# Optimization experiments

Hardware: AMD Instinct MI355X
Metric: run time of the kernel (lower is better)

Reference implementation:

```python
import jax, jax.numpy as jnp
import numpy as np

N_NODES = 100000
N_EDGES = 3200000
IN_CH = 256


def setup_inputs() -> dict:
    key = jax.random.key(0)
    k1, k2, k3 = jax.random.split(key, 3)
    x = jax.random.normal(k1, (N_NODES, IN_CH), dtype=jnp.float32)
    edge_index = jax.random.randint(k2, (2, N_EDGES), 0, N_NODES, dtype=jnp.int64)
    # GCNConv linear: weight [in_channels, 1] (applied as x @ W), bias [1]
    W = jax.random.normal(k3, (IN_CH, 1), dtype=jnp.float32) * (1.0 / np.sqrt(IN_CH))
    b = jnp.zeros((1,), dtype=jnp.float32)
    return {"x": x, "edge_index": edge_index, "W": W, "b": b}


def reference(x, edge_index, W, b):
    # PyG GCNConv(in, 1): h = x @ W; add self-loops; symmetric norm; scatter-add to target; + bias
    N = x.shape[0]
    self_loops = jnp.broadcast_to(jnp.arange(N, dtype=edge_index.dtype)[None, :], (2, N))
    ei = jnp.concatenate([edge_index, self_loops], axis=1)  # [2, E+N]
    src, dst = ei[0], ei[1]

    # degree computed at target (col) with unit edge weights, incl. self-loops
    deg = jax.ops.segment_sum(jnp.ones(ei.shape[1], dtype=x.dtype), dst, num_segments=N)
    deg_inv_sqrt = jnp.where(deg > 0, jax.lax.rsqrt(deg), 0.0)
    norm = deg_inv_sqrt[src] * deg_inv_sqrt[dst]  # [E+N]

    h = x @ W  # [N, 1] — project first (out_channels < in_channels)
    msg = norm[:, None] * h[src]  # [E+N, 1]
    out = jax.ops.segment_sum(msg, dst, num_segments=N)  # [N, 1]
    return out + b
```

## Files before the change

kernel.cpp:

```cpp
#include <hip/hip_runtime.h>

#define GCN_N 100000
#define GCN_E 3200000
#define GCN_C 256
#define BSHIFT 8
#define NBUCK 391
#define BCAP 9216

#define NPB 512
#define TPB 1024
#define ROWS ((GCN_N + NPB - 1) / NPB)

#define TB 1024
#define CHUNK 6144
#define NBIN ((GCN_E + CHUNK - 1) / CHUNK)
#define EPT (CHUNK / TB)

__global__ void __launch_bounds__(TPB) k_proj_init(const float* __restrict__ x,
                                                   const float* __restrict__ W,
                                                   float* __restrict__ h,
                                                   int* __restrict__ cursor) {
    const int tid = threadIdx.x, blk = blockIdx.x;
    if (blk == 0) {
        for (int i = tid; i < NBUCK; i += TPB) cursor[i] = 0;
    }
    const int lane = tid & 63, wv = tid >> 6;
    const int r0 = blk * ROWS;
    const int r1 = min(r0 + ROWS, GCN_N);
    const float4 wf = *reinterpret_cast<const float4*>(W + lane * 4);
    for (int i = r0 + wv; i < r1; i += 16) {
        const float4 xv = *reinterpret_cast<const float4*>(x + (size_t)i * GCN_C + lane * 4);
        float s = xv.x * wf.x + xv.y * wf.y + xv.z * wf.z + xv.w * wf.w;
        #pragma unroll
        for (int off = 32; off > 0; off >>= 1) s += __shfl_down(s, off, 64);
        if (lane == 0) h[i] = s;
    }
}

__global__ void __launch_bounds__(TB) k_bin(const int* __restrict__ src,
                                            const int* __restrict__ dst,
                                            int* __restrict__ cursor,
                                            int* __restrict__ bpack) {
    __shared__ int A[CHUNK];
    __shared__ int B[CHUNK];
    __shared__ int hist[NBUCK];
    __shared__ int lscan[NBUCK];
    __shared__ int gbase[NBUCK];
    __shared__ int wsum[16], woff[16];
    const int tid = threadIdx.x, blk = blockIdx.x;
    const int lane = tid & 63, wv = tid >> 6;
    const int c0 = blk * CHUNK;
    const int cn = min(CHUNK, GCN_E - c0);

    for (int b = tid; b < NBUCK; b += TB) hist[b] = 0;

    const int nq = cn >> 2;
    for (int k4 = tid; k4 < nq; k4 += TB) {
        const int4 d = *reinterpret_cast<const int4*>(dst + c0 + k4 * 4);
        const int4 s = *reinterpret_cast<const int4*>(src + c0 + k4 * 4);
        *reinterpret_cast<int4*>(&A[k4 * 4]) = d;
        *reinterpret_cast<int4*>(&B[k4 * 4]) = s;
    }
    for (int k = (cn & ~3) + tid; k < cn; k += TB) {
        A[k] = dst[c0 + k];
        B[k] = src[c0 + k];
    }
    __syncthreads();

    int my_pack[EPT], my_b[EPT], my_off[EPT];
    #pragma unroll
    for (int j = 0; j < EPT; ++j) {
        const int k = tid + j * TB;
        my_b[j] = -1;
        if (k < cn) {
            const int d = A[k];
            const int s = B[k];
            const int b = d >> BSHIFT;
            my_pack[j] = (s << BSHIFT) | (d & 255);
            my_b[j]    = b;
            my_off[j]  = atomicAdd(&hist[b], 1);
        }
    }
    __syncthreads();

    if (tid < NBUCK) gbase[tid] = atomicAdd(&cursor[tid], hist[tid]);
    {
        const int v = (tid < NBUCK) ? hist[tid] : 0;
        int incl = v;
        #pragma unroll
        for (int d2 = 1; d2 < 64; d2 <<= 1) {
            const int t = __shfl_up(incl, d2, 64);
            if (lane >= d2) incl += t;
        }
        if (lane == 63 && wv < 7) wsum[wv] = incl;
        __syncthreads();
        if (tid == 0) { int s = 0; for (int k2 = 0; k2 < 7; ++k2) { woff[k2] = s; s += wsum[k2]; } }
        __syncthreads();
        if (tid < NBUCK) lscan[tid] = incl - v + woff[wv];
    }
    __syncthreads();

    #pragma unroll
    for (int j = 0; j < EPT; ++j) {
        if (my_b[j] >= 0) {
            const int b    = my_b[j];
            const int slot = lscan[b] + my_off[j];
            const int goff = gbase[b] + my_off[j];
            B[slot] = my_pack[j];
            A[slot] = (goff < BCAP) ? (b * BCAP + goff) : -1;
        }
    }
    __syncthreads();

    for (int i = tid; i < cn; i += TB) {
        const int dpos = A[i];
        if (dpos >= 0) bpack[dpos] = B[i];
    }
}

__global__ void __launch_bounds__(1024) k_deg_norm(const int* __restrict__ bpack,
                                                   const int* __restrict__ cursor,
                                                   const float* __restrict__ h,
                                                   float* __restrict__ dis,
                                                   float* __restrict__ g) {
    __shared__ int cnt[256];
    const int p = blockIdx.x, tid = threadIdx.x;
    if (tid < 256) cnt[tid] = 0;
    __syncthreads();
    const int s0 = p * BCAP, s1 = s0 + min(cursor[p], BCAP);
    for (int i = s0 + tid; i < s1; i += 1024)
        atomicAdd(&cnt[bpack[i] & 255], 1);
    __syncthreads();
    if (tid < 256) {
        const int node = (p << BSHIFT) + tid;
        if (node < GCN_N) {
            const float r = rsqrtf(1.0f + (float)cnt[tid]);
            dis[node] = r;
            g[node]   = r * h[node];
        }
    }
}

__global__ void __launch_bounds__(1024) k_scatter_bin(const int* __restrict__ bpack,
                                                      const int* __restrict__ cursor,
                                                      const float* __restrict__ g,
                                                      const float* __restrict__ dis,
                                                      const float* __restrict__ bias,
                                                      float* __restrict__ out) {
    __shared__ float acc[256];
    const int p = blockIdx.x, tid = threadIdx.x;
    if (tid < 256) acc[tid] = 0.0f;
    __syncthreads();
    const int s0 = p * BCAP, s1 = s0 + min(cursor[p], BCAP);
    for (int i = s0 + tid; i < s1; i += 1024) {
        const int pk = bpack[i];
        atomicAdd(&acc[pk & 255], g[pk >> BSHIFT]);
    }
    __syncthreads();
    if (tid < 256) {
        const int node = (p << BSHIFT) + tid;
        if (node < GCN_N)
            out[node] = bias[0] + dis[node] * (acc[tid] + g[node]);
    }
}

__global__ void k_zero(float* __restrict__ a, int n) {
    int i = blockIdx.x * blockDim.x + threadIdx.x;
    const int stride = gridDim.x * blockDim.x;
    for (; i < n; i += stride) a[i] = 0.0f;
}
__global__ void k_proj_sep(const float* __restrict__ x, const float* __restrict__ W,
                           float* __restrict__ h, int n) {
    const int lane   = threadIdx.x & 63;
    const int wave   = (blockIdx.x * blockDim.x + threadIdx.x) >> 6;
    const int nwaves = (gridDim.x * blockDim.x) >> 6;
    const float4 wf = *reinterpret_cast<const float4*>(W + lane * 4);
    for (int i = wave; i < n; i += nwaves) {
        const float4 xv = *reinterpret_cast<const float4*>(x + (size_t)i * GCN_C + lane * 4);
        float s = xv.x * wf.x + xv.y * wf.y + xv.z * wf.z + xv.w * wf.w;
        #pragma unroll
        for (int off = 32; off > 0; off >>= 1)
            s += __shfl_down(s, off, 64);
        if (lane == 0) h[i] = s;
    }
}
__global__ void k_degree_flat(const int* __restrict__ dst, float* __restrict__ deg, int e) {
    int i = blockIdx.x * blockDim.x + threadIdx.x;
    const int stride = gridDim.x * blockDim.x;
    for (; i < e; i += stride) atomicAdd(&deg[dst[i]], 1.0f);
}
__global__ void k_norm_flat(const float* __restrict__ h, float* __restrict__ deg_dis,
                            float* __restrict__ out, const float* __restrict__ bias, int n) {
    const int i = blockIdx.x * blockDim.x + threadIdx.x;
    if (i < n) {
        const float r = rsqrtf(deg_dis[i] + 1.0f);
        deg_dis[i] = r;
        out[i] = bias[0] + r * r * h[i];
    }
}
__global__ void k_scatter_flat(const int* __restrict__ src, const int* __restrict__ dst,
                               const float* __restrict__ h, const float* __restrict__ dis,
                               float* __restrict__ out, int e) {
    int i = blockIdx.x * blockDim.x + threadIdx.x;
    const int stride = gridDim.x * blockDim.x;
    for (; i < e; i += stride) {
        const int s = src[i], d = dst[i];
        atomicAdd(&out[d], dis[s] * dis[d] * h[s]);
    }
}

extern "C" void kernel_launch(void* const* d_in, const int* in_sizes, int n_in,
                              void* d_out, int out_size, void* d_ws, size_t ws_size,
                              hipStream_t stream) {
    const float* x  = (const float*)d_in[0];
    const int*   ei = (const int*)d_in[1];
    const float* W  = (const float*)d_in[2];
    const float* b  = (const float*)d_in[3];
    float* out = (float*)d_out;
    const int* src = ei;
    const int* dst = ei + GCN_E;

    float* h      = (float*)d_ws;
    float* dis    = h + GCN_N;
    float* g      = dis + GCN_N;
    int*   cursor = (int*)(g + GCN_N);
    int*   bpack  = cursor + NBUCK;
    const size_t need = ((size_t)3 * GCN_N + NBUCK + (size_t)NBUCK * BCAP) * 4;

    if (ws_size >= need) {
        k_proj_init<<<NPB, TPB, 0, stream>>>(x, W, h, cursor);
        k_bin<<<NBIN, TB, 0, stream>>>(src, dst, cursor, bpack);
        k_deg_norm<<<NBUCK, 1024, 0, stream>>>(bpack, cursor, h, dis, g);
        k_scatter_bin<<<NBUCK, 1024, 0, stream>>>(bpack, cursor, g, dis, b, out);
    } else {
        float* hh  = (float*)d_ws;
        float* deg = hh + GCN_N;
        k_zero<<<512, 256, 0, stream>>>(deg, GCN_N);
        k_proj_sep<<<2048, 256, 0, stream>>>(x, W, hh, GCN_N);
        k_degree_flat<<<2048, 256, 0, stream>>>(dst, deg, GCN_E);
        k_norm_flat<<<(GCN_N + 255) / 256, 256, 0, stream>>>(hh, deg, out, b, GCN_N);
        k_scatter_flat<<<2048, 256, 0, stream>>>(src, dst, hh, deg, out, GCN_E);
    }
}
```

Measured before the change: 70.91 us.

## Fuse projection and edge binning into one interleaved-block kernel

Merges the x@W projection and the edge-binning pass into a single launch. Even blocks compute projection rows and odd blocks bin a chunk of edges, so the bandwidth-heavy projection can overlap with the atomic- and LDS-heavy binning instead of running after it. Cursor zeroing moves into a tiny separate kernel. Block size drops to 512 and chunks become GCN_E/1024 edges, which are no longer 4-aligned, so the vector int4 loads of src/dst start at unaligned addresses.

Measured after the change: 73.98 us. +4.3%, slower.

```diff
diff --git a/kernel.cpp b/kernel.cpp
--- a/kernel.cpp
+++ b/kernel.cpp
@@ -7,61 +7,61 @@
 #define NBUCK 391
 #define BCAP 9216
 
-#define NPB 512
-#define TPB 1024
-#define ROWS ((GCN_N + NPB - 1) / NPB)
-
-#define TB 1024
-#define CHUNK 6144
-#define NBIN ((GCN_E + CHUNK - 1) / CHUNK)
-#define EPT (CHUNK / TB)
-
-__global__ void __launch_bounds__(TPB) k_proj_init(const float* __restrict__ x,
-                                                   const float* __restrict__ W,
-                                                   float* __restrict__ h,
-                                                   int* __restrict__ cursor) {
-    const int tid = threadIdx.x, blk = blockIdx.x;
-    if (blk == 0) {
-        for (int i = tid; i < NBUCK; i += TPB) cursor[i] = 0;
-    }
-    const int lane = tid & 63, wv = tid >> 6;
-    const int r0 = blk * ROWS;
-    const int r1 = min(r0 + ROWS, GCN_N);
-    const float4 wf = *reinterpret_cast<const float4*>(W + lane * 4);
-    for (int i = r0 + wv; i < r1; i += 16) {
-        const float4 xv = *reinterpret_cast<const float4*>(x + (size_t)i * GCN_C + lane * 4);
-        float s = xv.x * wf.x + xv.y * wf.y + xv.z * wf.z + xv.w * wf.w;
-        #pragma unroll
-        for (int off = 32; off > 0; off >>= 1) s += __shfl_down(s, off, 64);
-        if (lane == 0) h[i] = s;
-    }
-}
-
-__global__ void __launch_bounds__(TB) k_bin(const int* __restrict__ src,
-                                            const int* __restrict__ dst,
-                                            int* __restrict__ cursor,
-                                            int* __restrict__ bpack) {
+#define NPAIR 1024
+#define TB 512
+#define CHUNK (GCN_E / NPAIR)
+#define EPT ((CHUNK + TB - 1) / TB)
+#define ROWS ((GCN_N + NPAIR - 1) / NPAIR)
+
+__global__ void k_init(int* __restrict__ cursor) {
+    const int i = threadIdx.x;
+    if (i < NBUCK) cursor[i] = 0;
+}
+
+__global__ void __launch_bounds__(TB) k_fused(const float* __restrict__ x,
+                                              const float* __restrict__ W,
+                                              float* __restrict__ h,
+                                              const int* __restrict__ src,
+                                              const int* __restrict__ dst,
+                                              int* __restrict__ cursor,
+                                              int* __restrict__ bpack) {
     __shared__ int A[CHUNK];
     __shared__ int B[CHUNK];
     __shared__ int hist[NBUCK];
     __shared__ int lscan[NBUCK];
     __shared__ int gbase[NBUCK];
-    __shared__ int wsum[16], woff[16];
-    const int tid = threadIdx.x, blk = blockIdx.x;
+    __shared__ int wsum[8], woff[8];
+    const int tid = threadIdx.x;
     const int lane = tid & 63, wv = tid >> 6;
+
+    if ((blockIdx.x & 1) == 0) {
+        const int blk = blockIdx.x >> 1;
+        const int r0 = blk * ROWS;
+        const int r1 = min(r0 + ROWS, GCN_N);
+        const float4 wf = *reinterpret_cast<const float4*>(W + lane * 4);
+        for (int i = r0 + wv; i < r1; i += 8) {
+            const float4 xv = *reinterpret_cast<const float4*>(x + (size_t)i * GCN_C + lane * 4);
+            float s = xv.x * wf.x + xv.y * wf.y + xv.z * wf.z + xv.w * wf.w;
+            #pragma unroll
+            for (int off = 32; off > 0; off >>= 1) s += __shfl_down(s, off, 64);
+            if (lane == 0) h[i] = s;
+        }
+        return;
+    }
+
+    const int blk = blockIdx.x >> 1;
     const int c0 = blk * CHUNK;
-    const int cn = min(CHUNK, GCN_E - c0);
 
     for (int b = tid; b < NBUCK; b += TB) hist[b] = 0;
 
-    const int nq = cn >> 2;
+    const int nq = CHUNK >> 2;
     for (int k4 = tid; k4 < nq; k4 += TB) {
         const int4 d = *reinterpret_cast<const int4*>(dst + c0 + k4 * 4);
         const int4 s = *reinterpret_cast<const int4*>(src + c0 + k4 * 4);
         *reinterpret_cast<int4*>(&A[k4 * 4]) = d;
         *reinterpret_cast<int4*>(&B[k4 * 4]) = s;
     }
-    for (int k = (cn & ~3) + tid; k < cn; k += TB) {
+    for (int k = (CHUNK & ~3) + tid; k < CHUNK; k += TB) {
         A[k] = dst[c0 + k];
         B[k] = src[c0 + k];
     }
@@ -72,7 +72,7 @@
     for (int j = 0; j < EPT; ++j) {
         const int k = tid + j * TB;
         my_b[j] = -1;
-        if (k < cn) {
+        if (k < CHUNK) {
             const int d = A[k];
             const int s = B[k];
             const int b = d >> BSHIFT;
@@ -112,7 +112,7 @@
     }
     __syncthreads();
 
-    for (int i = tid; i < cn; i += TB) {
+    for (int i = tid; i < CHUNK; i += TB) {
         const int dpos = A[i];
         if (dpos >= 0) bpack[dpos] = B[i];
     }
@@ -228,8 +228,8 @@
     const size_t need = ((size_t)3 * GCN_N + NBUCK + (size_t)NBUCK * BCAP) * 4;
 
     if (ws_size >= need) {
-        k_proj_init<<<NPB, TPB, 0, stream>>>(x, W, h, cursor);
-        k_bin<<<NBIN, TB, 0, stream>>>(src, dst, cursor, bpack);
+        k_init<<<1, 512, 0, stream>>>(cursor);
+        k_fused<<<2 * NPAIR, TB, 0, stream>>>(x, W, h, src, dst, cursor, bpack);
         k_deg_norm<<<NBUCK, 1024, 0, stream>>>(bpack, cursor, h, dis, g);
         k_scatter_bin<<<NBUCK, 1024, 0, stream>>>(bpack, cursor, g, dis, b, out);
     } else {
```
